# Performance work log

Measured on AMD Instinct MI355X. Metric: run time of the kernel, lower is better.

## Reference

```python
import jax, jax.numpy as jnp
import numpy as np

B, S, D, H = 2, 2048, 1024, 16
HD = D // H          # 64
HALF = HD // 2       # 32
EPS = 1e-6           # RMSNorm eps (module default eps=1e-6)


def setup_inputs() -> dict:
    key = jax.random.key(0)
    ks = jax.random.split(key, 6)
    x = jax.random.normal(ks[0], (B, S, D), jnp.float32)
    scale = 1.0 / np.sqrt(D)
    Wq = jax.random.normal(ks[1], (D, D), jnp.float32) * scale
    Wk = jax.random.normal(ks[2], (D, D), jnp.float32) * scale
    Wv = jax.random.normal(ks[3], (D, D), jnp.float32) * scale
    Wo = jax.random.normal(ks[4], (D, D), jnp.float32) * scale
    bq = jnp.zeros((D,), jnp.float32)
    bk = jnp.zeros((D,), jnp.float32)
    bv = jnp.zeros((D,), jnp.float32)
    bo = jnp.zeros((D,), jnp.float32)
    gq = jnp.ones((D,), jnp.float32)   # norm_q weight
    gk = jnp.ones((D,), jnp.float32)   # norm_k weight
    # Standard RoPE angles: pos * 10000^(-2i/head_dim); freqs = exp(i*ang)
    pos = jnp.arange(S, dtype=jnp.float32)
    inv_freq = 1.0 / (10000.0 ** (jnp.arange(0, HD, 2, dtype=jnp.float32) / HD))
    ang = pos[:, None] * inv_freq[None, :]          # (S, HALF)
    return dict(x=x, Wq=Wq, bq=bq, Wk=Wk, bk=bk, Wv=Wv, bv=bv, Wo=Wo, bo=bo,
                gq=gq, gk=gk, freqs_cos=jnp.cos(ang), freqs_sin=jnp.sin(ang))


def _rmsnorm(x, g):
    # x * rsqrt(mean(x^2) + eps) * g, computed in fp32 as in the torch module
    return x * jax.lax.rsqrt(jnp.mean(x * x, axis=-1, keepdims=True) + EPS) * g


def _rope(x, cos, sin):
    # x: (B,S,D) packed heads; rotate consecutive (even,odd) pairs per head.
    xr = x.reshape(B, S, H, HALF, 2)
    x0, x1 = xr[..., 0], xr[..., 1]
    c = cos[None, :, None, :]  # (1,S,1,HALF)
    s = sin[None, :, None, :]
    o0 = x0 * c - x1 * s
    o1 = x0 * s + x1 * c
    return jnp.stack([o0, o1], axis=-1).reshape(B, S, D)


def reference(x, Wq, bq, Wk, bk, Wv, bv, Wo, bo, gq, gk, freqs_cos, freqs_sin):
    q = _rmsnorm(x @ Wq.T + bq, gq)
    k = _rmsnorm(x @ Wk.T + bk, gk)
    v = x @ Wv.T + bv
    q = _rope(q, freqs_cos, freqs_sin)
    k = _rope(k, freqs_cos, freqs_sin)
    # SDPA (non-causal, as F.scaled_dot_product_attention default call)
    qh = q.reshape(B, S, H, HD)
    kh = k.reshape(B, S, H, HD)
    vh = v.reshape(B, S, H, HD)
    scores = jnp.einsum('bqhd,bkhd->bhqk', qh, kh) / np.sqrt(HD)
    attn = jax.nn.softmax(scores, axis=-1)
    out = jnp.einsum('bhqk,bkhd->bqhd', attn, vh).reshape(B, S, D)
    return out @ Wo.T + bo
```

## Files before the change

kernel.cpp:

```cpp
#include <hip/hip_runtime.h>

typedef unsigned short u16;
typedef unsigned int u32;
typedef u16 u16x4 __attribute__((ext_vector_type(4)));
typedef u16 u16x8 __attribute__((ext_vector_type(8)));
typedef u32 u32x2 __attribute__((ext_vector_type(2)));
typedef u32 u32x4 __attribute__((ext_vector_type(4)));
typedef float f32x4 __attribute__((ext_vector_type(4)));
typedef float f32x16 __attribute__((ext_vector_type(16)));
typedef __bf16 bf16x2 __attribute__((ext_vector_type(2)));
typedef __bf16 bf16x8 __attribute__((ext_vector_type(8)));

#define GLOAD16(gp, lp)                                             \
  __builtin_amdgcn_global_load_lds(                                 \
      (const __attribute__((address_space(1))) void*)(gp),          \
      (__attribute__((address_space(3))) void*)(lp), 16, 0, 0)

__device__ __forceinline__ u16 f2bf(float f) {
  unsigned int u = __builtin_bit_cast(unsigned int, f);
  u += 0x7FFFu + ((u >> 16) & 1u);
  return (u16)(u >> 16);
}
__device__ __forceinline__ float bf2f(u16 h) {
  return __builtin_bit_cast(float, (u32)h << 16);
}

__global__ __launch_bounds__(256) void f2b_kernel(const float* __restrict__ in,
                                                  u16* __restrict__ out, int n4) {
  int i = blockIdx.x * 256 + threadIdx.x;
  if (i < n4) {
    f32x4 v = *(const f32x4*)(in + (size_t)i * 4);
    u16x4 o;
    o[0] = f2bf(v[0]); o[1] = f2bf(v[1]); o[2] = f2bf(v[2]); o[3] = f2bf(v[3]);
    *(u16x4*)(out + (size_t)i * 4) = o;
  }
}

__global__ __launch_bounds__(256) void f2bw_kernel(const float* __restrict__ s0,
    const float* __restrict__ s1, const float* __restrict__ s2,
    const float* __restrict__ s3, u16* __restrict__ dst) {
  const int y = blockIdx.y;
  const float* s = (y == 0) ? s0 : ((y == 1) ? s1 : ((y == 2) ? s2 : s3));
  int i = blockIdx.x * 256 + threadIdx.x;
  f32x4 v = *(const f32x4*)(s + (size_t)i * 4);
  u16x4 o;
  o[0] = f2bf(v[0]); o[1] = f2bf(v[1]); o[2] = f2bf(v[2]); o[3] = f2bf(v[3]);
  *(u16x4*)(dst + (size_t)y * 1048576 + (size_t)i * 4) = o;
}

__device__ __forceinline__ void gemm_core(const u16* __restrict__ A,
                                          const u16* __restrict__ W,
                                          int bm0, int bn0,
                                          u16* ldsA, u16* ldsB,
                                          f32x4 acc[4][4]) {
  const int tid = threadIdx.x;
  const int l = tid & 63;
  const int lr = l & 15, lk = l >> 4;
  const int w = tid >> 6;
  const int wr = w >> 1, wc = w & 1;
  const int srow = tid >> 2, sko = (tid & 3) << 3;
  auto stage = [&](int kt, int buf) {
#pragma unroll
    for (int it = 0; it < 2; ++it) {
      int row = it * 64 + srow;
      GLOAD16(A + (size_t)(bm0 + row) * 1024 + kt * 32 + sko,
              ldsA + buf * 4096 + (it * 256 + tid) * 8);
      GLOAD16(W + (size_t)(bn0 + row) * 1024 + kt * 32 + sko,
              ldsB + buf * 4096 + (it * 256 + tid) * 8);
    }
  };
  stage(0, 0);
  stage(1, 1);
  int cur = 0, nx2 = 2;
  for (int kt = 0; kt < 32; ++kt) {
    if (kt < 31) asm volatile("s_waitcnt vmcnt(4)" ::: "memory");
    else         asm volatile("s_waitcnt vmcnt(0)" ::: "memory");
    __builtin_amdgcn_s_barrier();
    __builtin_amdgcn_sched_barrier(0);
    if (kt + 2 < 32) stage(kt + 2, nx2);
    const u16* lA = ldsA + cur * 4096;
    const u16* lB = ldsB + cur * 4096;
    bf16x8 af[4], bfr[4];
#pragma unroll
    for (int m = 0; m < 4; ++m)
      af[m] = *(const bf16x8*)(lA + (wr * 64 + m * 16 + lr) * 32 + lk * 8);
#pragma unroll
    for (int n = 0; n < 4; ++n)
      bfr[n] = *(const bf16x8*)(lB + (wc * 64 + n * 16 + lr) * 32 + lk * 8);
#pragma unroll
    for (int m = 0; m < 4; ++m)
#pragma unroll
      for (int n = 0; n < 4; ++n)
        acc[m][n] = __builtin_amdgcn_mfma_f32_16x16x32_bf16(af[m], bfr[n], acc[m][n], 0, 0, 0);
    cur = (cur == 2) ? 0 : cur + 1;
    nx2 = (nx2 == 2) ? 0 : nx2 + 1;
  }
}

__global__ __launch_bounds__(256) void qkv_gemm(const u16* __restrict__ xb,
    const u16* __restrict__ wq, const u16* __restrict__ wk, const u16* __restrict__ wv,
    const float* __restrict__ bq, const float* __restrict__ bk, const float* __restrict__ bv,
    u16* __restrict__ Qb, u16* __restrict__ Kb, u16* __restrict__ Vt) {
  __shared__ u16 ldsA[3 * 4096];
  __shared__ u16 ldsB[3 * 4096];
  const int z = blockIdx.z;
  const u16* W = (z == 0) ? wq : ((z == 1) ? wk : wv);
  const float* bias = (z == 0) ? bq : ((z == 1) ? bk : bv);
  const int bm0 = blockIdx.x * 128, bn0 = blockIdx.y * 128;
  const f32x4 zf = {0.f, 0.f, 0.f, 0.f};
  f32x4 acc[4][4];
#pragma unroll
  for (int m = 0; m < 4; ++m)
#pragma unroll
    for (int n = 0; n < 4; ++n) acc[m][n] = zf;
  gemm_core(xb, W, bm0, bn0, ldsA, ldsB, acc);
  const int tid = threadIdx.x, l = tid & 63, lr = l & 15, lk = l >> 4;
  const int w = tid >> 6, wr = w >> 1, wc = w & 1;
  float bcol[4];
#pragma unroll
  for (int n = 0; n < 4; ++n) bcol[n] = bias[bn0 + wc * 64 + n * 16 + lr];
  if (z < 2) {
    u16* outp = z ? Kb : Qb;
#pragma unroll
    for (int m = 0; m < 4; ++m)
#pragma unroll
      for (int n = 0; n < 4; ++n)
#pragma unroll
        for (int r = 0; r < 4; ++r) {
          int row = bm0 + wr * 64 + m * 16 + lk * 4 + r;
          int col = bn0 + wc * 64 + n * 16 + lr;
          outp[(size_t)row * 1024 + col] = f2bf(acc[m][n][r] + bcol[n]);
        }
  } else {
#pragma unroll
    for (int m = 0; m < 4; ++m)
#pragma unroll
      for (int n = 0; n < 4; ++n) {
        int row = bm0 + wr * 64 + m * 16 + lk * 4;
        int col = bn0 + wc * 64 + n * 16 + lr;
        int b = row >> 11, s = row & 2047, hh = col >> 6, hd = col & 63;
        u16x4 o;
#pragma unroll
        for (int r = 0; r < 4; ++r) o[r] = f2bf(acc[m][n][r] + bcol[n]);
        *(u16x4*)(Vt + (((size_t)((b * 16 + hh) * 64 + hd)) << 11) + s) = o;
      }
  }
}

__global__ __launch_bounds__(256) void proj_gemm(const u16* __restrict__ ctx,
    const u16* __restrict__ wo, const float* __restrict__ bo, float* __restrict__ out) {
  __shared__ u16 ldsA[3 * 4096];
  __shared__ u16 ldsB[3 * 4096];
  const int bm0 = blockIdx.x * 128, bn0 = blockIdx.y * 128;
  const f32x4 zf = {0.f, 0.f, 0.f, 0.f};
  f32x4 acc[4][4];
#pragma unroll
  for (int m = 0; m < 4; ++m)
#pragma unroll
    for (int n = 0; n < 4; ++n) acc[m][n] = zf;
  gemm_core(ctx, wo, bm0, bn0, ldsA, ldsB, acc);
  const int tid = threadIdx.x, l = tid & 63, lr = l & 15, lk = l >> 4;
  const int w = tid >> 6, wr = w >> 1, wc = w & 1;
  float bcol[4];
#pragma unroll
  for (int n = 0; n < 4; ++n) bcol[n] = bo[bn0 + wc * 64 + n * 16 + lr];
#pragma unroll
  for (int m = 0; m < 4; ++m)
#pragma unroll
    for (int n = 0; n < 4; ++n)
#pragma unroll
      for (int r = 0; r < 4; ++r) {
        int row = bm0 + wr * 64 + m * 16 + lk * 4 + r;
        int col = bn0 + wc * 64 + n * 16 + lr;
        out[(size_t)row * 1024 + col] = acc[m][n][r] + bcol[n];
      }
}

__global__ __launch_bounds__(256) void rmsrope(const u16* __restrict__ Qb,
    const u16* __restrict__ Kb, const float* __restrict__ gq, const float* __restrict__ gk,
    const float* __restrict__ fc, const float* __restrict__ fs,
    u16* __restrict__ Qh, u16* __restrict__ Kh) {
  const int row = blockIdx.x;
  const int which = blockIdx.y;
  const u16* src = (which ? Kb : Qb) + (size_t)row * 1024;
  const float* g = which ? gk : gq;
  u16* dst = which ? Kh : Qh;
  const int t = threadIdx.x;
  u16x4 raw = *(const u16x4*)(src + t * 4);
  float v0 = bf2f(raw[0]), v1 = bf2f(raw[1]), v2 = bf2f(raw[2]), v3 = bf2f(raw[3]);
  float ss = v0 * v0 + v1 * v1 + v2 * v2 + v3 * v3;
#pragma unroll
  for (int mm = 1; mm < 64; mm <<= 1) ss += __shfl_xor(ss, mm);
  __shared__ float red[4];
  if ((t & 63) == 0) red[t >> 6] = ss;
  __syncthreads();
  float rstd = rsqrtf((red[0] + red[1] + red[2] + red[3]) * (1.0f / 1024.0f) + 1e-6f);
  if (!which) rstd *= 0.18033688011112042f;
  int d = t * 4, hh = d >> 6, dh = d & 63, p = dh >> 1;
  int s = row & 2047, b = row >> 11;
  float c0 = fc[(s << 5) + p], s0 = fs[(s << 5) + p];
  float c1 = fc[(s << 5) + p + 1], s1 = fs[(s << 5) + p + 1];
  float x0 = v0 * rstd * g[d];
  float x1 = v1 * rstd * g[d + 1];
  float x2 = v2 * rstd * g[d + 2];
  float x3 = v3 * rstd * g[d + 3];
  u16x4 o;
  o[0] = f2bf(x0 * c0 - x1 * s0);
  o[1] = f2bf(x0 * s0 + x1 * c0);
  o[2] = f2bf(x2 * c1 - x3 * s1);
  o[3] = f2bf(x2 * s1 + x3 * c1);
  *(u16x4*)(dst + ((size_t)((b << 4) + hh) * 2048 + s) * 64 + dh) = o;
}

__global__ __launch_bounds__(256, 2) void attn_kernel(const u16* __restrict__ Qh,
    const u16* __restrict__ Kh, const u16* __restrict__ Vt, u16* __restrict__ ctx) {
  __shared__ u16 Kbuf[3][4096];
  __shared__ u16 Vbuf[3][4096];
  const int tid = threadIdx.x;
  const int w = tid >> 6, l = tid & 63;
  const int lq = l & 31, hi = l >> 5;
  const bool hiB = (hi != 0);
  const int id = blockIdx.x;
  const int qt = (id >> 3) & 15;
  const int hb = (id & 7) | ((id >> 7) << 3);
  const int h = hb & 15, b = hb >> 4;
  const int bh = b * 16 + h;
  const u16* Q = Qh + (size_t)bh * 2048 * 64;
  const u16* K = Kh + (size_t)bh * 2048 * 64;
  const u16* V = Vt + (size_t)bh * 64 * 2048;
  const int q0 = qt * 128 + w * 32;
  bf16x8 qf[4];
#pragma unroll
  for (int hs = 0; hs < 4; ++hs)
    qf[hs] = *(const bf16x8*)(Q + (size_t)(q0 + lq) * 64 + hs * 16 + hi * 8);
  auto stage = [&](int kb, int buf) {
#pragma unroll
    for (int it = 0; it < 2; ++it) {
      int c = it * 256 + tid;
      int row = c >> 3, gc = (c & 7) ^ (row & 7);
      GLOAD16(K + ((size_t)(kb * 64 + row) << 6) + gc * 8, &Kbuf[buf][c * 8]);
      GLOAD16(V + ((size_t)row << 11) + kb * 64 + gc * 8, &Vbuf[buf][c * 8]);
    }
  };
  const f32x16 z16 = {0,0,0,0, 0,0,0,0, 0,0,0,0, 0,0,0,0};
  f32x16 O0 = z16, O1 = z16;
  float Mrun = -1e30f, lsum = 0.f;
  stage(0, 0);
  stage(1, 1);
  int cur = 0, nx2 = 2;
  for (int kb = 0; kb < 32; ++kb) {
    if (kb < 31) asm volatile("s_waitcnt vmcnt(4)" ::: "memory");
    else         asm volatile("s_waitcnt vmcnt(0)" ::: "memory");
    __builtin_amdgcn_s_barrier();
    __builtin_amdgcn_sched_barrier(0);
    if (kb + 2 < 32) stage(kb + 2, nx2);
    const u16* Kb_ = &Kbuf[cur][0];
    const u16* Vb_ = &Vbuf[cur][0];
    f32x16 sc0 = z16, sc1 = z16;
    __builtin_amdgcn_s_setprio(1);
#pragma unroll
    for (int hs = 0; hs < 4; ++hs) {
      int ch = (hs * 2 + hi) ^ (lq & 7);
      bf16x8 k0 = *(const bf16x8*)(Kb_ + (lq * 8 + ch) * 8);
      bf16x8 k1 = *(const bf16x8*)(Kb_ + ((32 + lq) * 8 + ch) * 8);
      sc0 = __builtin_amdgcn_mfma_f32_32x32x16_bf16(k0, qf[hs], sc0, 0, 0, 0);
      sc1 = __builtin_amdgcn_mfma_f32_32x32x16_bf16(k1, qf[hs], sc1, 0, 0, 0);
    }
    __builtin_amdgcn_s_setprio(0);
    float bm = sc0[0];
#pragma unroll
    for (int i = 1; i < 16; ++i) bm = fmaxf(bm, sc0[i]);
#pragma unroll
    for (int i = 0; i < 16; ++i) bm = fmaxf(bm, sc1[i]);
    bm = fmaxf(bm, __shfl_xor(bm, 32));
    if (!__all(bm <= Mrun + 1.4427f)) {
      float nM = fmaxf(Mrun, bm);
      float f = exp2f(Mrun - nM);
      lsum *= f;
#pragma unroll
      for (int i = 0; i < 16; ++i) { O0[i] *= f; O1[i] *= f; }
      Mrun = nM;
    }
    float rs = 0.f;
    u32 pk0[8], pk1[8];
#pragma unroll
    for (int m = 0; m < 8; ++m) {
      float a0 = exp2f(sc0[2 * m] - Mrun), a1 = exp2f(sc0[2 * m + 1] - Mrun);
      float c0 = exp2f(sc1[2 * m] - Mrun), c1 = exp2f(sc1[2 * m + 1] - Mrun);
      rs += (a0 + a1) + (c0 + c1);
      bf16x2 pA; pA[0] = (__bf16)a0; pA[1] = (__bf16)a1;
      bf16x2 pC; pC[0] = (__bf16)c0; pC[1] = (__bf16)c1;
      pk0[m] = __builtin_bit_cast(u32, pA);
      pk1[m] = __builtin_bit_cast(u32, pC);
    }
    rs += __shfl_xor(rs, 32);
    lsum += rs;
    auto xchg = [&](u32 X, u32 Y, u32& wlo, u32& whi) {
      u32 s1 = hiB ? X : Y;
      u32 r = (u32)__shfl_xor((int)s1, 32);
      wlo = hiB ? r : X;
      whi = hiB ? Y : r;
    };
    bf16x8 pb[4];
    {
      u32 w0, w1, w2, w3;
      xchg(pk0[0], pk0[2], w0, w2);
      xchg(pk0[1], pk0[3], w1, w3);
      u32x4 pw = {w0, w1, w2, w3};
      pb[0] = __builtin_bit_cast(bf16x8, pw);
      xchg(pk0[4], pk0[6], w0, w2);
      xchg(pk0[5], pk0[7], w1, w3);
      u32x4 pw1 = {w0, w1, w2, w3};
      pb[1] = __builtin_bit_cast(bf16x8, pw1);
      xchg(pk1[0], pk1[2], w0, w2);
      xchg(pk1[1], pk1[3], w1, w3);
      u32x4 pw2 = {w0, w1, w2, w3};
      pb[2] = __builtin_bit_cast(bf16x8, pw2);
      xchg(pk1[4], pk1[6], w0, w2);
      xchg(pk1[5], pk1[7], w1, w3);
      u32x4 pw3 = {w0, w1, w2, w3};
      pb[3] = __builtin_bit_cast(bf16x8, pw3);
    }
    __builtin_amdgcn_s_setprio(1);
#pragma unroll
    for (int ks = 0; ks < 4; ++ks) {
      int cv = (ks * 2 + hi) ^ (lq & 7);
      bf16x8 v0 = *(const bf16x8*)(Vb_ + (lq * 8 + cv) * 8);
      bf16x8 v1 = *(const bf16x8*)(Vb_ + ((32 + lq) * 8 + cv) * 8);
      O0 = __builtin_amdgcn_mfma_f32_32x32x16_bf16(v0, pb[ks], O0, 0, 0, 0);
      O1 = __builtin_amdgcn_mfma_f32_32x32x16_bf16(v1, pb[ks], O1, 0, 0, 0);
    }
    __builtin_amdgcn_s_setprio(0);
    cur = (cur == 2) ? 0 : cur + 1;
    nx2 = (nx2 == 2) ? 0 : nx2 + 1;
  }
  float inv = 1.0f / lsum;
  const size_t rowoff = ((size_t)(b * 2048 + q0 + lq)) * 1024 + h * 64;
#pragma unroll
  for (int g = 0; g < 4; ++g) {
    u16x4 oa, ob;
#pragma unroll
    for (int rr = 0; rr < 4; ++rr) {
      oa[rr] = f2bf(O0[4 * g + rr] * inv);
      ob[rr] = f2bf(O1[4 * g + rr] * inv);
    }
    *(u16x4*)(ctx + rowoff + 8 * g + 4 * hi) = oa;
    *(u16x4*)(ctx + rowoff + 32 + 8 * g + 4 * hi) = ob;
  }
}

extern "C" void kernel_launch(void* const* d_in, const int* in_sizes, int n_in,
                              void* d_out, int out_size, void* d_ws, size_t ws_size,
                              hipStream_t stream) {
  (void)in_sizes; (void)n_in; (void)out_size; (void)ws_size;
  const float* x  = (const float*)d_in[0];
  const float* Wq = (const float*)d_in[1];
  const float* bq = (const float*)d_in[2];
  const float* Wk = (const float*)d_in[3];
  const float* bk = (const float*)d_in[4];
  const float* Wv = (const float*)d_in[5];
  const float* bv = (const float*)d_in[6];
  const float* Wo = (const float*)d_in[7];
  const float* bo = (const float*)d_in[8];
  const float* gq = (const float*)d_in[9];
  const float* gk = (const float*)d_in[10];
  const float* fc = (const float*)d_in[11];
  const float* fs = (const float*)d_in[12];
  float* out = (float*)d_out;
  char* ws = (char*)d_ws;
  u16*  xb  = (u16*)(ws + 0);
  u16*  wqb = (u16*)(ws + 8388608);
  u16*  wkb = (u16*)(ws + 10485760);
  u16*  wvb = (u16*)(ws + 12582912);
  u16*  wob = (u16*)(ws + 14680064);
  u16*  Qfb = (u16*)(ws + 16777216);
  u16*  Kfb = (u16*)(ws + 25165824);
  u16*  Qhb = (u16*)(ws + 33554432);
  u16*  Khb = (u16*)(ws + 41943040);
  u16*  Vtb = (u16*)(ws + 50331648);
  u16*  ctx = (u16*)(ws + 58720256);

  f2b_kernel<<<4096, 256, 0, stream>>>(x, xb, 1048576);
  f2bw_kernel<<<dim3(1024, 4), 256, 0, stream>>>(Wq, Wk, Wv, Wo, wqb);
  qkv_gemm<<<dim3(32, 8, 3), 256, 0, stream>>>(xb, wqb, wkb, wvb, bq, bk, bv, Qfb, Kfb, Vtb);
  rmsrope<<<dim3(4096, 2), 256, 0, stream>>>(Qfb, Kfb, gq, gk, fc, fs, Qhb, Khb);
  attn_kernel<<<512, 256, 0, stream>>>(Qhb, Khb, Vtb, ctx);
  proj_gemm<<<dim3(32, 8), 256, 0, stream>>>(ctx, wob, bo, out);
}
```

Measured before the change: 148.1 us.

## Software-pipeline QK^T of next tile with softmax/PV of current tile

Restructures the attention loop so the QK^T MFMAs for key block t+1 are issued before the softmax and PV of block t, using two score register sets in a ping-pong unrolled-by-two loop. Shared-memory staging goes from triple to quad buffering so K for the next tile is resident early. The aim is to overlap MFMA work with the exp/shuffle softmax phase. In exchange it raises register pressure (an extra 32-float score set) and LDS use (64KB per block), which could hurt occupancy at two blocks per CU.

```diff
diff --git a/kernel.cpp b/kernel.cpp
--- a/kernel.cpp
+++ b/kernel.cpp
@@ -214,8 +214,8 @@
 
 __global__ __launch_bounds__(256, 2) void attn_kernel(const u16* __restrict__ Qh,
     const u16* __restrict__ Kh, const u16* __restrict__ Vt, u16* __restrict__ ctx) {
-  __shared__ u16 Kbuf[3][4096];
-  __shared__ u16 Vbuf[3][4096];
+  __shared__ u16 Kbuf[4][4096];
+  __shared__ u16 Vbuf[4][4096];
   const int tid = threadIdx.x;
   const int w = tid >> 6, l = tid & 63;
   const int lq = l & 31, hi = l >> 5;
@@ -245,28 +245,22 @@
   const f32x16 z16 = {0,0,0,0, 0,0,0,0, 0,0,0,0, 0,0,0,0};
   f32x16 O0 = z16, O1 = z16;
   float Mrun = -1e30f, lsum = 0.f;
-  stage(0, 0);
-  stage(1, 1);
-  int cur = 0, nx2 = 2;
-  for (int kb = 0; kb < 32; ++kb) {
-    if (kb < 31) asm volatile("s_waitcnt vmcnt(4)" ::: "memory");
-    else         asm volatile("s_waitcnt vmcnt(0)" ::: "memory");
-    __builtin_amdgcn_s_barrier();
-    __builtin_amdgcn_sched_barrier(0);
-    if (kb + 2 < 32) stage(kb + 2, nx2);
-    const u16* Kb_ = &Kbuf[cur][0];
-    const u16* Vb_ = &Vbuf[cur][0];
-    f32x16 sc0 = z16, sc1 = z16;
+
+  auto qk_step = [&](const u16* Kb_, f32x16& s0, f32x16& s1) {
+    s0 = z16; s1 = z16;
     __builtin_amdgcn_s_setprio(1);
 #pragma unroll
     for (int hs = 0; hs < 4; ++hs) {
       int ch = (hs * 2 + hi) ^ (lq & 7);
       bf16x8 k0 = *(const bf16x8*)(Kb_ + (lq * 8 + ch) * 8);
       bf16x8 k1 = *(const bf16x8*)(Kb_ + ((32 + lq) * 8 + ch) * 8);
-      sc0 = __builtin_amdgcn_mfma_f32_32x32x16_bf16(k0, qf[hs], sc0, 0, 0, 0);
-      sc1 = __builtin_amdgcn_mfma_f32_32x32x16_bf16(k1, qf[hs], sc1, 0, 0, 0);
+      s0 = __builtin_amdgcn_mfma_f32_32x32x16_bf16(k0, qf[hs], s0, 0, 0, 0);
+      s1 = __builtin_amdgcn_mfma_f32_32x32x16_bf16(k1, qf[hs], s1, 0, 0, 0);
     }
     __builtin_amdgcn_s_setprio(0);
+  };
+
+  auto sm_pv = [&](const u16* Vb_, f32x16& sc0, f32x16& sc1) {
     float bm = sc0[0];
 #pragma unroll
     for (int i = 1; i < 16; ++i) bm = fmaxf(bm, sc0[i]);
@@ -296,8 +290,8 @@
     rs += __shfl_xor(rs, 32);
     lsum += rs;
     auto xchg = [&](u32 X, u32 Y, u32& wlo, u32& whi) {
-      u32 s1 = hiB ? X : Y;
-      u32 r = (u32)__shfl_xor((int)s1, 32);
+      u32 s1v = hiB ? X : Y;
+      u32 r = (u32)__shfl_xor((int)s1v, 32);
       wlo = hiB ? r : X;
       whi = hiB ? Y : r;
     };
@@ -331,8 +325,39 @@
       O1 = __builtin_amdgcn_mfma_f32_32x32x16_bf16(v1, pb[ks], O1, 0, 0, 0);
     }
     __builtin_amdgcn_s_setprio(0);
-    cur = (cur == 2) ? 0 : cur + 1;
-    nx2 = (nx2 == 2) ? 0 : nx2 + 1;
+  };
+
+  stage(0, 0);
+  stage(1, 1);
+  stage(2, 2);
+  asm volatile("s_waitcnt vmcnt(8)" ::: "memory");
+  __builtin_amdgcn_s_barrier();
+  __builtin_amdgcn_sched_barrier(0);
+  f32x16 scA0, scA1, scB0, scB1;
+  qk_step(&Kbuf[0][0], scA0, scA1);
+
+  int t = 0;
+  for (int dt = 0; dt < 16; ++dt) {
+    {
+      if (t < 30) asm volatile("s_waitcnt vmcnt(4)" ::: "memory");
+      else        asm volatile("s_waitcnt vmcnt(0)" ::: "memory");
+      __builtin_amdgcn_s_barrier();
+      __builtin_amdgcn_sched_barrier(0);
+      if (t + 3 < 32) stage(t + 3, (t + 3) & 3);
+      qk_step(&Kbuf[(t + 1) & 3][0], scB0, scB1);
+      sm_pv(&Vbuf[t & 3][0], scA0, scA1);
+      ++t;
+    }
+    {
+      if (t < 30) asm volatile("s_waitcnt vmcnt(4)" ::: "memory");
+      else        asm volatile("s_waitcnt vmcnt(0)" ::: "memory");
+      __builtin_amdgcn_s_barrier();
+      __builtin_amdgcn_sched_barrier(0);
+      if (t + 3 < 32) stage(t + 3, (t + 3) & 3);
+      if (t < 31) qk_step(&Kbuf[(t + 1) & 3][0], scA0, scA1);
+      sm_pv(&Vbuf[t & 3][0], scB0, scB1);
+      ++t;
+    }
   }
   float inv = 1.0f / lsum;
   const size_t rowoff = ((size_t)(b * 2048 + q0 + lq)) * 1024 + h * 64;
```

Result: no change. 147.6 us (-0.4%).

## Store Q/K/V in MFMA fragment order and load attention operands directly to registers

Applied to the files above, without the earlier changes.

The QKV GEMM and RMSNorm/RoPE kernels now write Q, K and V in a pre-swizzled fragment layout, so each lane's MFMA operand is a contiguous 16-byte chunk. The attention kernel drops its LDS staging, barriers and async global-to-LDS copies, and instead loads K/V fragments straight into registers with register double-buffering across key tiles. This removes LDS traffic and block-wide synchronisation, but the four waves of a block now each fetch the same K/V from global memory/cache, and register pressure rises from holding two K/V tile buffers.

```diff
diff --git a/kernel.cpp b/kernel.cpp
--- a/kernel.cpp
+++ b/kernel.cpp
@@ -4,7 +4,6 @@
 typedef unsigned int u32;
 typedef u16 u16x4 __attribute__((ext_vector_type(4)));
 typedef u16 u16x8 __attribute__((ext_vector_type(8)));
-typedef u32 u32x2 __attribute__((ext_vector_type(2)));
 typedef u32 u32x4 __attribute__((ext_vector_type(4)));
 typedef float f32x4 __attribute__((ext_vector_type(4)));
 typedef float f32x16 __attribute__((ext_vector_type(16)));
@@ -100,7 +99,7 @@
 __global__ __launch_bounds__(256) void qkv_gemm(const u16* __restrict__ xb,
     const u16* __restrict__ wq, const u16* __restrict__ wk, const u16* __restrict__ wv,
     const float* __restrict__ bq, const float* __restrict__ bk, const float* __restrict__ bv,
-    u16* __restrict__ Qb, u16* __restrict__ Kb, u16* __restrict__ Vt) {
+    u16* __restrict__ Qb, u16* __restrict__ Kb, u16* __restrict__ Vf) {
   __shared__ u16 ldsA[3 * 4096];
   __shared__ u16 ldsB[3 * 4096];
   const int z = blockIdx.z;
@@ -138,11 +137,17 @@
       for (int n = 0; n < 4; ++n) {
         int row = bm0 + wr * 64 + m * 16 + lk * 4;
         int col = bn0 + wc * 64 + n * 16 + lr;
-        int b = row >> 11, s = row & 2047, hh = col >> 6, hd = col & 63;
+        int b = row >> 11, sf = row & 2047, hh = col >> 6, hd = col & 63;
+        int t = sf >> 6, kin = sf & 63;
+        int ks = kin >> 4, hiv = (kin >> 3) & 1, j0 = kin & 7;
+        int vhalf = hd >> 5, lq = hd & 31;
         u16x4 o;
 #pragma unroll
         for (int r = 0; r < 4; ++r) o[r] = f2bf(acc[m][n][r] + bcol[n]);
-        *(u16x4*)(Vt + (((size_t)((b * 16 + hh) * 64 + hd)) << 11) + s) = o;
+        size_t addr = (size_t)(b * 16 + hh) * 131072 +
+                      (size_t)(((t * 4 + ks) * 2 + vhalf)) * 512 +
+                      ((hiv << 5) + lq) * 8 + j0;
+        *(u16x4*)(Vf + addr) = o;
       }
   }
 }
@@ -179,12 +184,11 @@
 __global__ __launch_bounds__(256) void rmsrope(const u16* __restrict__ Qb,
     const u16* __restrict__ Kb, const float* __restrict__ gq, const float* __restrict__ gk,
     const float* __restrict__ fc, const float* __restrict__ fs,
-    u16* __restrict__ Qh, u16* __restrict__ Kh) {
+    u16* __restrict__ Qf, u16* __restrict__ Kf) {
   const int row = blockIdx.x;
   const int which = blockIdx.y;
   const u16* src = (which ? Kb : Qb) + (size_t)row * 1024;
   const float* g = which ? gk : gq;
-  u16* dst = which ? Kh : Qh;
   const int t = threadIdx.x;
   u16x4 raw = *(const u16x4*)(src + t * 4);
   float v0 = bf2f(raw[0]), v1 = bf2f(raw[1]), v2 = bf2f(raw[2]), v3 = bf2f(raw[3]);
@@ -209,13 +213,20 @@
   o[1] = f2bf(x0 * s0 + x1 * c0);
   o[2] = f2bf(x2 * c1 - x3 * s1);
   o[3] = f2bf(x2 * s1 + x3 * c1);
-  *(u16x4*)(dst + ((size_t)((b << 4) + hh) * 2048 + s) * 64 + dh) = o;
-}
-
-__global__ __launch_bounds__(256, 2) void attn_kernel(const u16* __restrict__ Qh,
-    const u16* __restrict__ Kh, const u16* __restrict__ Vt, u16* __restrict__ ctx) {
-  __shared__ u16 Kbuf[3][4096];
-  __shared__ u16 Vbuf[3][4096];
+  const size_t base = (size_t)(b * 16 + hh) * 131072;
+  const int hs = dh >> 4, hi = (dh >> 3) & 1, j0 = dh & 7;
+  size_t addr;
+  if (!which) {
+    addr = base + (size_t)((s >> 5) * 4 + hs) * 512 + ((hi << 5) + (s & 31)) * 8 + j0;
+  } else {
+    addr = base + (size_t)(((s >> 6) * 4 + hs) * 2 + ((s >> 5) & 1)) * 512 +
+           ((hi << 5) + (s & 31)) * 8 + j0;
+  }
+  *(u16x4*)((which ? Kf : Qf) + addr) = o;
+}
+
+__global__ __launch_bounds__(256, 2) void attn_kernel(const u16* __restrict__ Qf,
+    const u16* __restrict__ Kf, const u16* __restrict__ Vf, u16* __restrict__ ctx) {
   const int tid = threadIdx.x;
   const int w = tid >> 6, l = tid & 63;
   const int lq = l & 31, hi = l >> 5;
@@ -225,48 +236,41 @@
   const int hb = (id & 7) | ((id >> 7) << 3);
   const int h = hb & 15, b = hb >> 4;
   const int bh = b * 16 + h;
-  const u16* Q = Qh + (size_t)bh * 2048 * 64;
-  const u16* K = Kh + (size_t)bh * 2048 * 64;
-  const u16* V = Vt + (size_t)bh * 64 * 2048;
-  const int q0 = qt * 128 + w * 32;
+  const u16* Qp = Qf + (size_t)bh * 131072;
+  const u16* Kp = Kf + (size_t)bh * 131072;
+  const u16* Vp = Vf + (size_t)bh * 131072;
   bf16x8 qf[4];
 #pragma unroll
   for (int hs = 0; hs < 4; ++hs)
-    qf[hs] = *(const bf16x8*)(Q + (size_t)(q0 + lq) * 64 + hs * 16 + hi * 8);
-  auto stage = [&](int kb, int buf) {
-#pragma unroll
-    for (int it = 0; it < 2; ++it) {
-      int c = it * 256 + tid;
-      int row = c >> 3, gc = (c & 7) ^ (row & 7);
-      GLOAD16(K + ((size_t)(kb * 64 + row) << 6) + gc * 8, &Kbuf[buf][c * 8]);
-      GLOAD16(V + ((size_t)row << 11) + kb * 64 + gc * 8, &Vbuf[buf][c * 8]);
-    }
+    qf[hs] = *(const bf16x8*)(Qp + (size_t)((qt * 4 + w) * 4 + hs) * 512 + l * 8);
+
+  auto ldK = [&](int t, bf16x8* kr) {
+#pragma unroll
+    for (int i = 0; i < 8; ++i)
+      kr[i] = *(const bf16x8*)(Kp + ((size_t)t * 8 + i) * 512 + l * 8);
   };
+  auto ldV = [&](int t, bf16x8* vr) {
+#pragma unroll
+    for (int i = 0; i < 8; ++i)
+      vr[i] = *(const bf16x8*)(Vp + ((size_t)t * 8 + i) * 512 + l * 8);
+  };
+
   const f32x16 z16 = {0,0,0,0, 0,0,0,0, 0,0,0,0, 0,0,0,0};
   f32x16 O0 = z16, O1 = z16;
   float Mrun = -1e30f, lsum = 0.f;
-  stage(0, 0);
-  stage(1, 1);
-  int cur = 0, nx2 = 2;
-  for (int kb = 0; kb < 32; ++kb) {
-    if (kb < 31) asm volatile("s_waitcnt vmcnt(4)" ::: "memory");
-    else         asm volatile("s_waitcnt vmcnt(0)" ::: "memory");
-    __builtin_amdgcn_s_barrier();
-    __builtin_amdgcn_sched_barrier(0);
-    if (kb + 2 < 32) stage(kb + 2, nx2);
-    const u16* Kb_ = &Kbuf[cur][0];
-    const u16* Vb_ = &Vbuf[cur][0];
-    f32x16 sc0 = z16, sc1 = z16;
+
+  auto qk_step = [&](const bf16x8* kr, f32x16& s0, f32x16& s1) {
+    s0 = z16; s1 = z16;
     __builtin_amdgcn_s_setprio(1);
 #pragma unroll
     for (int hs = 0; hs < 4; ++hs) {
-      int ch = (hs * 2 + hi) ^ (lq & 7);
-      bf16x8 k0 = *(const bf16x8*)(Kb_ + (lq * 8 + ch) * 8);
-      bf16x8 k1 = *(const bf16x8*)(Kb_ + ((32 + lq) * 8 + ch) * 8);
-      sc0 = __builtin_amdgcn_mfma_f32_32x32x16_bf16(k0, qf[hs], sc0, 0, 0, 0);
-      sc1 = __builtin_amdgcn_mfma_f32_32x32x16_bf16(k1, qf[hs], sc1, 0, 0, 0);
+      s0 = __builtin_amdgcn_mfma_f32_32x32x16_bf16(kr[hs * 2 + 0], qf[hs], s0, 0, 0, 0);
+      s1 = __builtin_amdgcn_mfma_f32_32x32x16_bf16(kr[hs * 2 + 1], qf[hs], s1, 0, 0, 0);
     }
     __builtin_amdgcn_s_setprio(0);
+  };
+
+  auto sm_pv = [&](const bf16x8* vr, f32x16& sc0, f32x16& sc1) {
     float bm = sc0[0];
 #pragma unroll
     for (int i = 1; i < 16; ++i) bm = fmaxf(bm, sc0[i]);
@@ -296,8 +300,8 @@
     rs += __shfl_xor(rs, 32);
     lsum += rs;
     auto xchg = [&](u32 X, u32 Y, u32& wlo, u32& whi) {
-      u32 s1 = hiB ? X : Y;
-      u32 r = (u32)__shfl_xor((int)s1, 32);
+      u32 s1v = hiB ? X : Y;
+      u32 r = (u32)__shfl_xor((int)s1v, 32);
       wlo = hiB ? r : X;
       whi = hiB ? Y : r;
     };
@@ -324,17 +328,33 @@
     __builtin_amdgcn_s_setprio(1);
 #pragma unroll
     for (int ks = 0; ks < 4; ++ks) {
-      int cv = (ks * 2 + hi) ^ (lq & 7);
-      bf16x8 v0 = *(const bf16x8*)(Vb_ + (lq * 8 + cv) * 8);
-      bf16x8 v1 = *(const bf16x8*)(Vb_ + ((32 + lq) * 8 + cv) * 8);
-      O0 = __builtin_amdgcn_mfma_f32_32x32x16_bf16(v0, pb[ks], O0, 0, 0, 0);
-      O1 = __builtin_amdgcn_mfma_f32_32x32x16_bf16(v1, pb[ks], O1, 0, 0, 0);
+      O0 = __builtin_amdgcn_mfma_f32_32x32x16_bf16(vr[ks * 2 + 0], pb[ks], O0, 0, 0, 0);
+      O1 = __builtin_amdgcn_mfma_f32_32x32x16_bf16(vr[ks * 2 + 1], pb[ks], O1, 0, 0, 0);
     }
     __builtin_amdgcn_s_setprio(0);
-    cur = (cur == 2) ? 0 : cur + 1;
-    nx2 = (nx2 == 2) ? 0 : nx2 + 1;
+  };
+
+  bf16x8 kA[8], kB[8], vA[8], vB[8];
+  f32x16 scX0, scX1;
+  ldK(0, kA);
+  ldV(0, vA);
+#pragma unroll 1
+  for (int dt = 0; dt < 16; ++dt) {
+    int t = dt * 2;
+    {
+      ldK(t + 1, kB);
+      ldV(t + 1, vB);
+      qk_step(kA, scX0, scX1);
+      sm_pv(vA, scX0, scX1);
+    }
+    {
+      if (dt < 15) { ldK(t + 2, kA); ldV(t + 2, vA); }
+      qk_step(kB, scX0, scX1);
+      sm_pv(vB, scX0, scX1);
+    }
   }
   float inv = 1.0f / lsum;
+  const int q0 = qt * 128 + w * 32;
   const size_t rowoff = ((size_t)(b * 2048 + q0 + lq)) * 1024 + h * 64;
 #pragma unroll
   for (int g = 0; g < 4; ++g) {
@@ -375,15 +395,15 @@
   u16*  wob = (u16*)(ws + 14680064);
   u16*  Qfb = (u16*)(ws + 16777216);
   u16*  Kfb = (u16*)(ws + 25165824);
-  u16*  Qhb = (u16*)(ws + 33554432);
-  u16*  Khb = (u16*)(ws + 41943040);
-  u16*  Vtb = (u16*)(ws + 50331648);
+  u16*  Qfr = (u16*)(ws + 33554432);
+  u16*  Kfr = (u16*)(ws + 41943040);
+  u16*  Vfr = (u16*)(ws + 50331648);
   u16*  ctx = (u16*)(ws + 58720256);
 
   f2b_kernel<<<4096, 256, 0, stream>>>(x, xb, 1048576);
   f2bw_kernel<<<dim3(1024, 4), 256, 0, stream>>>(Wq, Wk, Wv, Wo, wqb);
-  qkv_gemm<<<dim3(32, 8, 3), 256, 0, stream>>>(xb, wqb, wkb, wvb, bq, bk, bv, Qfb, Kfb, Vtb);
-  rmsrope<<<dim3(4096, 2), 256, 0, stream>>>(Qfb, Kfb, gq, gk, fc, fs, Qhb, Khb);
-  attn_kernel<<<512, 256, 0, stream>>>(Qhb, Khb, Vtb, ctx);
+  qkv_gemm<<<dim3(32, 8, 3), 256, 0, stream>>>(xb, wqb, wkb, wvb, bq, bk, bv, Qfb, Kfb, Vfr);
+  rmsrope<<<dim3(4096, 2), 256, 0, stream>>>(Qfb, Kfb, gq, gk, fc, fs, Qfr, Kfr);
+  attn_kernel<<<512, 256, 0, stream>>>(Qfr, Kfr, Vfr, ctx);
   proj_gemm<<<dim3(32, 8), 256, 0, stream>>>(ctx, wob, bo, out);
 }
```

Result: no change. 149.4 us (+0.8%).
